# Kernel tuning notes

Hardware: AMD Instinct MI355X
Metric: run time of the kernel (lower is better)

Reference implementation:

```python
import jax, jax.numpy as jnp
import numpy as np

N_EMBD = 1024
N_HEAD = 16
HEAD_DIM = N_EMBD // N_HEAD
B, T = 4, 2048


def setup_inputs() -> dict:
    key = jax.random.key(0)
    ks = jax.random.split(key, 5)
    s_in = 1.0 / np.sqrt(N_EMBD)
    return {
        "x": jax.random.normal(ks[0], (B, T, N_EMBD), dtype=jnp.float32),
        "w_attn": jax.random.normal(ks[1], (N_EMBD, 3 * N_EMBD), dtype=jnp.float32) * s_in,
        "b_attn": jnp.zeros((3 * N_EMBD,), dtype=jnp.float32),
        "w_proj": jax.random.normal(ks[2], (N_EMBD, N_EMBD), dtype=jnp.float32) * s_in,
        "b_proj": jnp.zeros((N_EMBD,), dtype=jnp.float32),
    }


def reference(x, w_attn, b_attn, w_proj, b_proj):
    b, t, c = x.shape
    qkv = x @ w_attn + b_attn                      # [B,T,3C]
    q, k, v = jnp.split(qkv, 3, axis=-1)
    # [B,T,C] -> [B,H,T,D]
    def heads(z):
        return z.reshape(b, t, N_HEAD, HEAD_DIM).transpose(0, 2, 1, 3)
    q, k, v = heads(q), heads(k), heads(v)
    scale = 1.0 / np.sqrt(HEAD_DIM)
    att = jnp.einsum("bhqd,bhkd->bhqk", q, k) * scale
    causal = jnp.tril(jnp.ones((t, t), dtype=bool))
    att = jnp.where(causal, att, -jnp.inf)
    att = jax.nn.softmax(att, axis=-1)
    y = jnp.einsum("bhqk,bhkd->bhqd", att, v)      # [B,H,T,D]
    y = y.transpose(0, 2, 1, 3).reshape(b, t, c)
    return y @ w_proj + b_proj
```

## Files before the change

kernel.cpp:

```cpp
#include <hip/hip_runtime.h>
#include <hip/hip_bf16.h>

#define B_  4
#define T_  2048
#define C_  1024
#define H_  16
#define D_  64
#define C3_ 3072

typedef __attribute__((ext_vector_type(8))) short bf16x8;
typedef __attribute__((ext_vector_type(4))) float f32x4;
typedef unsigned short u16;

#define CSCALE 0.1803368801111204f

__device__ __forceinline__ u16 f2bf(float f) {
  union { float f; unsigned int u; } v; v.f = f;
  unsigned int r = (v.u + 0x7FFFu + ((v.u >> 16) & 1u)) >> 16;
  return (u16)r;
}

__device__ __forceinline__ void gload16(void* l, const void* g) {
  __builtin_amdgcn_global_load_lds(
      (const __attribute__((address_space(1))) unsigned int*)g,
      (__attribute__((address_space(3))) unsigned int*)l, 16, 0, 0);
}

__global__ __launch_bounds__(256)
void cvt_bf16(const float* __restrict__ in, u16* __restrict__ out, int n8) {
  int i = blockIdx.x * 256 + threadIdx.x;
  if (i >= n8) return;
  float4 a = *(const float4*)(in + (size_t)i * 8);
  float4 b = *(const float4*)(in + (size_t)i * 8 + 4);
  ushort4 lo, hi;
  lo.x = f2bf(a.x); lo.y = f2bf(a.y); lo.z = f2bf(a.z); lo.w = f2bf(a.w);
  hi.x = f2bf(b.x); hi.y = f2bf(b.y); hi.z = f2bf(b.z); hi.w = f2bf(b.w);
  *(ushort4*)(out + (size_t)i * 8) = lo;
  *(ushort4*)(out + (size_t)i * 8 + 4) = hi;
}

__global__ __launch_bounds__(256)
void transcvt(const float* __restrict__ w, u16* __restrict__ wT, int K, int N) {
  int n  = blockIdx.x * 64 + (threadIdx.x & 63);
  int k0 = blockIdx.y * 16 + (threadIdx.x >> 6) * 4;
  float v0 = w[(size_t)(k0 + 0) * N + n];
  float v1 = w[(size_t)(k0 + 1) * N + n];
  float v2 = w[(size_t)(k0 + 2) * N + n];
  float v3 = w[(size_t)(k0 + 3) * N + n];
  ushort4 o; o.x = f2bf(v0); o.y = f2bf(v1); o.z = f2bf(v2); o.w = f2bf(v3);
  *(ushort4*)(wT + (size_t)n * K + k0) = o;
}

__global__ __launch_bounds__(256)
void vtrans(const u16* __restrict__ qkv, u16* __restrict__ vT) {
  const int bid = blockIdx.x;
  const int bh = bid >> 6, tc = bid & 63;
  const int d = threadIdx.x & 63, t4 = threadIdx.x >> 6;
  const int t8 = tc * 4 + t4;
  const int b = bh >> 4, h = bh & 15;
  const u16* src = qkv + (size_t)(b * T_ + t8 * 8) * C3_ + 2 * C_ + h * 64 + d;
  union { u16 a[8]; int4 v; } u;
#pragma unroll
  for (int e = 0; e < 8; ++e) u.a[e] = src[(size_t)e * C3_];
  *(int4*)(vT + ((size_t)bh * 64 + d) * T_ + t8 * 8) = u.v;
}

template <typename OutT>
__global__ __launch_bounds__(256)
void gemm_bf16(const u16* __restrict__ A, const u16* __restrict__ Bt,
               const float* __restrict__ bias, OutT* __restrict__ C,
               int M, int N, int K, int qscale_cols) {
  __shared__ int4 As4[512];
  __shared__ int4 Bs4[512];

  const int tid  = threadIdx.x;
  const int lane = tid & 63;
  const int wid  = tid >> 6;
  const int wr   = wid >> 1, wc = wid & 1;
  const int row0 = blockIdx.y * 128, col0 = blockIdx.x * 128;

  f32x4 acc[4][4];
#pragma unroll
  for (int m = 0; m < 4; ++m)
#pragma unroll
    for (int n = 0; n < 4; ++n) acc[m][n] = (f32x4){0.f, 0.f, 0.f, 0.f};

  const int L1 = tid, L2 = 256 + tid;
  const u16* a1 = A + (size_t)(row0 + ((L1 >> 6) * 16) + (L1 & 15)) * K + ((L1 >> 4) & 3) * 8;
  const u16* a2 = A + (size_t)(row0 + ((L2 >> 6) * 16) + (L2 & 15)) * K + ((L2 >> 4) & 3) * 8;
  const u16* b1 = Bt + (size_t)(col0 + ((L1 >> 6) * 16) + (L1 & 15)) * K + ((L1 >> 4) & 3) * 8;
  const u16* b2 = Bt + (size_t)(col0 + ((L2 >> 6) * 16) + (L2 & 15)) * K + ((L2 >> 4) & 3) * 8;

  const int nk = K >> 5;
  for (int kt = 0; kt < nk; ++kt) {
    __syncthreads();
    gload16(As4 + wid * 64, a1);
    gload16(As4 + 256 + wid * 64, a2);
    gload16(Bs4 + wid * 64, b1);
    gload16(Bs4 + 256 + wid * 64, b2);
    a1 += 32; a2 += 32; b1 += 32; b2 += 32;
    __syncthreads();

    bf16x8 a[4], b[4];
#pragma unroll
    for (int m = 0; m < 4; ++m)
      a[m] = *(const bf16x8*)(As4 + (wr * 4 + m) * 64 + lane);
#pragma unroll
    for (int n = 0; n < 4; ++n)
      b[n] = *(const bf16x8*)(Bs4 + (wc * 4 + n) * 64 + lane);
#pragma unroll
    for (int m = 0; m < 4; ++m)
#pragma unroll
      for (int n = 0; n < 4; ++n)
        acc[m][n] = __builtin_amdgcn_mfma_f32_16x16x32_bf16(a[m], b[n], acc[m][n], 0, 0, 0);
  }

  const int cc = lane & 15, qg = lane >> 4;
#pragma unroll
  for (int m = 0; m < 4; ++m) {
#pragma unroll
    for (int n = 0; n < 4; ++n) {
      const int gc = col0 + wc * 64 + n * 16 + cc;
      const float bv = bias[gc];
      const float sc = (gc < qscale_cols) ? CSCALE : 1.0f;
#pragma unroll
      for (int r = 0; r < 4; ++r) {
        const int gr = row0 + wr * 64 + m * 16 + qg * 4 + r;
        float val = (acc[m][n][r] + bv) * sc;
        if constexpr (sizeof(OutT) == 2)
          ((u16*)C)[(size_t)gr * N + gc] = f2bf(val);
        else
          ((float*)C)[(size_t)gr * N + gc] = val;
      }
    }
  }
}

__global__ __launch_bounds__(512, 4)
void attn_mfma(const u16* __restrict__ qkv, const u16* __restrict__ vT,
               u16* __restrict__ yout) {
  __shared__ int4 Ks4[512];
  __shared__ int4 Vs4[512];
  __shared__ int4 Ps4[2048];

  const int n   = blockIdx.x;
  const int xcd = n & 7, t = n >> 3;
  const int bh  = xcd * 8 + (t >> 3);
  const int ip  = t & 7;
  const int b   = bh >> 4, h = bh & 15;

  const int tid = threadIdx.x;
  const int lane = tid & 63, wq = tid >> 6;
  const int sub = wq & 3;
  const int cc = lane & 15, qg = lane >> 4;

  const int qt128 = (wq < 4) ? ip : (15 - ip);
  const int qrow0 = qt128 * 128 + sub * 32;
  const int diag  = qt128 * 2 + (sub >> 1);
  const int jn    = 32 - 2 * ip;

  const u16* kbase = qkv + (size_t)b * T_ * C3_ + C_ + h * D_;
  const u16* vtb   = vT + (size_t)bh * D_ * T_;

  bf16x8 qf[2][2];
#pragma unroll
  for (int hf = 0; hf < 2; ++hf) {
    const u16* qb = qkv + (size_t)(b * T_ + qrow0 + hf * 16 + cc) * C3_ + h * D_;
    qf[hf][0] = *(const bf16x8*)(qb + qg * 8);
    qf[hf][1] = *(const bf16x8*)(qb + 32 + qg * 8);
  }

  const u16* kg = kbase + (size_t)((tid >> 7) * 16 + (tid & 15)) * C3_ +
                  ((tid >> 6) & 1) * 32 + ((tid >> 4) & 3) * 8;
  const u16* vg = vtb + (size_t)((tid >> 7) * 16 + (tid & 15)) * T_ +
                  ((tid >> 6) & 1) * 32 + ((tid >> 4) & 3) * 8;

  int4 kpref = *(const int4*)kg;
  int4 vpref = *(const int4*)vg;

  float m_r[2] = {-1e30f, -1e30f}, l_r[2] = {0.f, 0.f};
  f32x4 o[2][4];
#pragma unroll
  for (int hf = 0; hf < 2; ++hf)
#pragma unroll
    for (int db = 0; db < 4; ++db) o[hf][db] = (f32x4){0.f, 0.f, 0.f, 0.f};

  for (int j = 0; j < jn; ++j) {
    __syncthreads();
    Ks4[tid] = kpref;
    Vs4[tid] = vpref;
    __syncthreads();
    if (j + 1 < jn) {
      kpref = *(const int4*)(kg + (size_t)(j + 1) * 64 * C3_);
      vpref = *(const int4*)(vg + (j + 1) * 64);
    }
    if (j > diag) continue;

    __builtin_amdgcn_s_setprio(1);
    f32x4 s[2][4];
#pragma unroll
    for (int kb = 0; kb < 4; ++kb) {
      bf16x8 kf0 = *(const bf16x8*)(Ks4 + kb * 128 + lane);
      bf16x8 kf1 = *(const bf16x8*)(Ks4 + kb * 128 + 64 + lane);
#pragma unroll
      for (int hf = 0; hf < 2; ++hf) {
        f32x4 z = (f32x4){0.f, 0.f, 0.f, 0.f};
        z = __builtin_amdgcn_mfma_f32_16x16x32_bf16(kf0, qf[hf][0], z, 0, 0, 0);
        z = __builtin_amdgcn_mfma_f32_16x16x32_bf16(kf1, qf[hf][1], z, 0, 0, 0);
        s[hf][kb] = z;
      }
    }
    __builtin_amdgcn_s_setprio(0);

    if (j == diag) {
#pragma unroll
      for (int hf = 0; hf < 2; ++hf) {
        const int qabs = qrow0 + hf * 16 + cc;
#pragma unroll
        for (int kb = 0; kb < 4; ++kb)
#pragma unroll
          for (int r = 0; r < 4; ++r)
            if ((j * 64 + kb * 16 + qg * 4 + r) > qabs) s[hf][kb][r] = -1e30f;
      }
    }

#pragma unroll
    for (int hf = 0; hf < 2; ++hf) {
      float mx = s[hf][0][0];
#pragma unroll
      for (int kb = 0; kb < 4; ++kb)
#pragma unroll
        for (int r = 0; r < 4; ++r) mx = fmaxf(mx, s[hf][kb][r]);
      mx = fmaxf(mx, __shfl_xor(mx, 16));
      mx = fmaxf(mx, __shfl_xor(mx, 32));

      if (!__all(mx <= m_r[hf])) {
        float mn = fmaxf(m_r[hf], mx);
        float al = exp2f(m_r[hf] - mn);
        m_r[hf] = mn;
        l_r[hf] *= al;
        float alq[4];
#pragma unroll
        for (int r = 0; r < 4; ++r)
          alq[r] = __shfl(al, (lane & 48) | (qg * 4 + r));
#pragma unroll
        for (int db = 0; db < 4; ++db)
#pragma unroll
          for (int r = 0; r < 4; ++r) o[hf][db][r] *= alq[r];
      }

      float lsum = 0.f;
#pragma unroll
      for (int kb = 0; kb < 4; ++kb)
#pragma unroll
        for (int r = 0; r < 4; ++r) {
          float p = exp2f(s[hf][kb][r] - m_r[hf]);
          s[hf][kb][r] = p;
          lsum += p;
        }
      l_r[hf] += lsum;

      char* myPb = (char*)(Ps4 + wq * 256 + hf * 128);
#pragma unroll
      for (int kb = 0; kb < 4; ++kb) {
        unsigned plo, phi;
        asm("v_cvt_pk_bf16_f32 %0, %1, %2" : "=v"(plo) : "v"(s[hf][kb][0]), "v"(s[hf][kb][1]));
        asm("v_cvt_pk_bf16_f32 %0, %1, %2" : "=v"(phi) : "v"(s[hf][kb][2]), "v"(s[hf][kb][3]));
        const int kv0 = kb * 16 + qg * 4;
        const int g = ((kv0 >> 5) << 6) + (((kv0 >> 3) & 3) << 4) + cc;
        uint2 pk; pk.x = plo; pk.y = phi;
        *(uint2*)(myPb + g * 16 + (kv0 & 7) * 2) = pk;
      }
    }

    bf16x8 pa[2][2];
#pragma unroll
    for (int hf = 0; hf < 2; ++hf)
#pragma unroll
      for (int ks = 0; ks < 2; ++ks)
        pa[hf][ks] = *(const bf16x8*)(Ps4 + wq * 256 + hf * 128 + ks * 64 + lane);
    __builtin_amdgcn_s_setprio(1);
#pragma unroll
    for (int db = 0; db < 4; ++db) {
#pragma unroll
      for (int ks = 0; ks < 2; ++ks) {
        bf16x8 vf = *(const bf16x8*)(Vs4 + db * 128 + ks * 64 + lane);
        o[0][db] = __builtin_amdgcn_mfma_f32_16x16x32_bf16(pa[0][ks], vf, o[0][db], 0, 0, 0);
        o[1][db] = __builtin_amdgcn_mfma_f32_16x16x32_bf16(pa[1][ks], vf, o[1][db], 0, 0, 0);
      }
    }
    __builtin_amdgcn_s_setprio(0);
  }

#pragma unroll
  for (int hf = 0; hf < 2; ++hf) {
    float ls = l_r[hf];
    ls += __shfl_xor(ls, 16);
    ls += __shfl_xor(ls, 32);
    float linv_l = 1.0f / ls;
    float linv[4];
#pragma unroll
    for (int r = 0; r < 4; ++r)
      linv[r] = __shfl(linv_l, (lane & 48) | (qg * 4 + r));

    u16* yb = yout + (size_t)(b * T_ + qrow0 + hf * 16 + qg * 4) * C_ + h * D_ + cc;
#pragma unroll
    for (int db = 0; db < 4; ++db)
#pragma unroll
      for (int r = 0; r < 4; ++r)
        yb[(size_t)r * C_ + db * 16] = f2bf(o[hf][db][r] * linv[r]);
  }
}

extern "C" void kernel_launch(void* const* d_in, const int* in_sizes, int n_in,
                              void* d_out, int out_size, void* d_ws, size_t ws_size,
                              hipStream_t stream) {
  const float* x      = (const float*)d_in[0];
  const float* w_attn = (const float*)d_in[1];
  const float* b_attn = (const float*)d_in[2];
  const float* w_proj = (const float*)d_in[3];
  const float* b_proj = (const float*)d_in[4];
  float* out = (float*)d_out;

  char* ws = (char*)d_ws;
  u16* xb  = (u16*)(ws);
  u16* waT = (u16*)(ws + 16777216);
  u16* wpT = (u16*)(ws + 23068672);
  u16* qkv = (u16*)(ws + 25165824);
  u16* yb  = (u16*)(ws + 75497472);
  u16* vT  = (u16*)(ws + 92274688);

  cvt_bf16<<<4096, 256, 0, stream>>>(x, xb, (B_ * T_ * C_) / 8);
  transcvt<<<dim3(C3_ / 64, C_ / 16), 256, 0, stream>>>(w_attn, waT, C_, C3_);
  transcvt<<<dim3(C_ / 64, C_ / 16), 256, 0, stream>>>(w_proj, wpT, C_, C_);

  gemm_bf16<u16><<<dim3(C3_ / 128, (B_ * T_) / 128), 256, 0, stream>>>(
      xb, waT, b_attn, qkv, B_ * T_, C3_, C_, C_);

  vtrans<<<4096, 256, 0, stream>>>(qkv, vT);

  attn_mfma<<<dim3(8 * H_ * B_), 512, 0, stream>>>(qkv, vT, yb);

  gemm_bf16<float><<<dim3(C_ / 128, (B_ * T_) / 128), 256, 0, stream>>>(
      yb, wpT, b_proj, out, B_ * T_, C_, C_, 0);
}
```

Before: 248.1 us.

## Replace 128x128 GEMM with double-buffered 256x256 ping-pong pipelined GEMM

```diff
diff --git a/kernel.cpp b/kernel.cpp
--- a/kernel.cpp
+++ b/kernel.cpp
@@ -66,67 +66,201 @@
 }
 
 template <typename OutT>
-__global__ __launch_bounds__(256)
-void gemm_bf16(const u16* __restrict__ A, const u16* __restrict__ Bt,
-               const float* __restrict__ bias, OutT* __restrict__ C,
-               int M, int N, int K, int qscale_cols) {
-  __shared__ int4 As4[512];
-  __shared__ int4 Bs4[512];
-
-  const int tid  = threadIdx.x;
-  const int lane = tid & 63;
-  const int wid  = tid >> 6;
-  const int wr   = wid >> 1, wc = wid & 1;
-  const int row0 = blockIdx.y * 128, col0 = blockIdx.x * 128;
-
-  f32x4 acc[4][4];
-#pragma unroll
-  for (int m = 0; m < 4; ++m)
-#pragma unroll
-    for (int n = 0; n < 4; ++n) acc[m][n] = (f32x4){0.f, 0.f, 0.f, 0.f};
-
-  const int L1 = tid, L2 = 256 + tid;
-  const u16* a1 = A + (size_t)(row0 + ((L1 >> 6) * 16) + (L1 & 15)) * K + ((L1 >> 4) & 3) * 8;
-  const u16* a2 = A + (size_t)(row0 + ((L2 >> 6) * 16) + (L2 & 15)) * K + ((L2 >> 4) & 3) * 8;
-  const u16* b1 = Bt + (size_t)(col0 + ((L1 >> 6) * 16) + (L1 & 15)) * K + ((L1 >> 4) & 3) * 8;
-  const u16* b2 = Bt + (size_t)(col0 + ((L2 >> 6) * 16) + (L2 & 15)) * K + ((L2 >> 4) & 3) * 8;
-
-  const int nk = K >> 5;
-  for (int kt = 0; kt < nk; ++kt) {
-    __syncthreads();
-    gload16(As4 + wid * 64, a1);
-    gload16(As4 + 256 + wid * 64, a2);
-    gload16(Bs4 + wid * 64, b1);
-    gload16(Bs4 + 256 + wid * 64, b2);
-    a1 += 32; a2 += 32; b1 += 32; b2 += 32;
-    __syncthreads();
-
-    bf16x8 a[4], b[4];
-#pragma unroll
-    for (int m = 0; m < 4; ++m)
-      a[m] = *(const bf16x8*)(As4 + (wr * 4 + m) * 64 + lane);
-#pragma unroll
-    for (int n = 0; n < 4; ++n)
-      b[n] = *(const bf16x8*)(Bs4 + (wc * 4 + n) * 64 + lane);
-#pragma unroll
-    for (int m = 0; m < 4; ++m)
-#pragma unroll
-      for (int n = 0; n < 4; ++n)
-        acc[m][n] = __builtin_amdgcn_mfma_f32_16x16x32_bf16(a[m], b[n], acc[m][n], 0, 0, 0);
+__global__ __launch_bounds__(512, 2)
+void gemm256(const u16* __restrict__ A, const u16* __restrict__ Bt,
+             const float* __restrict__ bias, OutT* __restrict__ C,
+             int M, int N, int K, int qscale_cols) {
+  __shared__ int4 lds[8192];
+
+  const int tid = threadIdx.x, lane = tid & 63, wid = tid >> 6;
+  const int wr = wid >> 2, wc = wid & 3;
+  const int row0 = blockIdx.y * 256, col0 = blockIdx.x * 256;
+
+  f32x4 acc[8][4];
+#pragma unroll
+  for (int m = 0; m < 8; ++m)
+#pragma unroll
+    for (int nf = 0; nf < 4; ++nf) acc[m][nf] = (f32x4){0.f, 0.f, 0.f, 0.f};
+
+  const u16* pA[2][2]; const u16* pB[2][2];
+#pragma unroll
+  for (int h = 0; h < 2; ++h)
+#pragma unroll
+    for (int i = 0; i < 2; ++i) {
+      int g = h * 1024 + i * 512 + tid;
+      int rr = ((g >> 7) << 4) + (g & 15), ko = ((g >> 4) & 7) * 8;
+      pA[h][i] = A + (size_t)(row0 + rr) * K + ko;
+      pB[h][i] = Bt + (size_t)(col0 + rr) * K + ko;
+    }
+
+  auto stage = [&](int t, int isA, int h, int buf) {
+    const u16* p0 = (isA ? pA[h][0] : pB[h][0]) + t * 64;
+    const u16* p1 = (isA ? pA[h][1] : pB[h][1]) + t * 64;
+    int4* d = &lds[buf * 4096 + (isA ? 0 : 2048) + h * 1024 + wid * 64];
+    gload16(d, p0);
+    gload16(d + 512, p1);
+  };
+  auto rdA = [&](int f, int kk, int buf) {
+    return *(const bf16x8*)&lds[buf * 4096 + (wr * 8 + f) * 128 + kk * 64 + lane];
+  };
+  auto rdB = [&](int nf, int kk, int buf) {
+    return *(const bf16x8*)&lds[buf * 4096 + 2048 + (wc * 4 + nf) * 128 + kk * 64 + lane];
+  };
+
+  const int nk = K >> 6, nit = nk >> 1;
+
+  stage(0, 1, 0, 0); stage(0, 1, 1, 0); stage(0, 0, 0, 0); stage(0, 0, 1, 0);
+  stage(1, 0, 0, 1); stage(1, 0, 1, 1); stage(1, 1, 0, 1);
+  asm volatile("s_waitcnt vmcnt(6)" ::: "memory");
+  __builtin_amdgcn_s_barrier();
+
+  for (int it = 0; it < nit; ++it) {
+    const int t1g = 2 * it + 1, t2g = t1g + 1, t3g = t1g + 2;
+    bf16x8 a0[4][2], a1[4][2], b0[2][2], b1[2][2];
+
+#pragma unroll
+    for (int m = 0; m < 4; ++m) { a0[m][0] = rdA(m, 0, 0); a0[m][1] = rdA(m, 1, 0); }
+#pragma unroll
+    for (int nf = 0; nf < 2; ++nf) { b0[nf][0] = rdB(nf, 0, 0); b0[nf][1] = rdB(nf, 1, 0); }
+    stage(t1g, 1, 1, 1);
+    __builtin_amdgcn_s_barrier();
+    __builtin_amdgcn_s_setprio(1);
+#pragma unroll
+    for (int m = 0; m < 4; ++m)
+#pragma unroll
+      for (int nf = 0; nf < 2; ++nf) {
+        acc[m][nf] = __builtin_amdgcn_mfma_f32_16x16x32_bf16(a0[m][0], b0[nf][0], acc[m][nf], 0, 0, 0);
+        acc[m][nf] = __builtin_amdgcn_mfma_f32_16x16x32_bf16(a0[m][1], b0[nf][1], acc[m][nf], 0, 0, 0);
+      }
+    __builtin_amdgcn_s_setprio(0);
+    __builtin_amdgcn_s_barrier();
+
+#pragma unroll
+    for (int nf = 0; nf < 2; ++nf) { b1[nf][0] = rdB(2 + nf, 0, 0); b1[nf][1] = rdB(2 + nf, 1, 0); }
+    __builtin_amdgcn_s_barrier();
+    __builtin_amdgcn_s_setprio(1);
+#pragma unroll
+    for (int m = 0; m < 4; ++m)
+#pragma unroll
+      for (int nf = 0; nf < 2; ++nf) {
+        acc[m][2 + nf] = __builtin_amdgcn_mfma_f32_16x16x32_bf16(a0[m][0], b1[nf][0], acc[m][2 + nf], 0, 0, 0);
+        acc[m][2 + nf] = __builtin_amdgcn_mfma_f32_16x16x32_bf16(a0[m][1], b1[nf][1], acc[m][2 + nf], 0, 0, 0);
+      }
+    __builtin_amdgcn_s_setprio(0);
+    __builtin_amdgcn_s_barrier();
+
+#pragma unroll
+    for (int m = 0; m < 4; ++m) { a1[m][0] = rdA(4 + m, 0, 0); a1[m][1] = rdA(4 + m, 1, 0); }
+    if (t2g < nk) stage(t2g, 0, 0, 0);
+    __builtin_amdgcn_s_barrier();
+    __builtin_amdgcn_s_setprio(1);
+#pragma unroll
+    for (int m = 0; m < 4; ++m)
+#pragma unroll
+      for (int nf = 0; nf < 2; ++nf) {
+        acc[4 + m][2 + nf] = __builtin_amdgcn_mfma_f32_16x16x32_bf16(a1[m][0], b1[nf][0], acc[4 + m][2 + nf], 0, 0, 0);
+        acc[4 + m][2 + nf] = __builtin_amdgcn_mfma_f32_16x16x32_bf16(a1[m][1], b1[nf][1], acc[4 + m][2 + nf], 0, 0, 0);
+      }
+    __builtin_amdgcn_s_setprio(0);
+    __builtin_amdgcn_s_barrier();
+
+    if (t2g < nk) {
+      stage(t2g, 0, 1, 0);
+      stage(t2g, 1, 0, 0);
+      asm volatile("s_waitcnt vmcnt(6)" ::: "memory");
+    } else {
+      asm volatile("s_waitcnt vmcnt(0)" ::: "memory");
+    }
+    __builtin_amdgcn_s_barrier();
+    __builtin_amdgcn_s_setprio(1);
+#pragma unroll
+    for (int m = 0; m < 4; ++m)
+#pragma unroll
+      for (int nf = 0; nf < 2; ++nf) {
+        acc[4 + m][nf] = __builtin_amdgcn_mfma_f32_16x16x32_bf16(a1[m][0], b0[nf][0], acc[4 + m][nf], 0, 0, 0);
+        acc[4 + m][nf] = __builtin_amdgcn_mfma_f32_16x16x32_bf16(a1[m][1], b0[nf][1], acc[4 + m][nf], 0, 0, 0);
+      }
+    __builtin_amdgcn_s_setprio(0);
+    __builtin_amdgcn_s_barrier();
+
+#pragma unroll
+    for (int m = 0; m < 4; ++m) { a0[m][0] = rdA(m, 0, 1); a0[m][1] = rdA(m, 1, 1); }
+#pragma unroll
+    for (int nf = 0; nf < 2; ++nf) { b0[nf][0] = rdB(nf, 0, 1); b0[nf][1] = rdB(nf, 1, 1); }
+    if (t2g < nk) stage(t2g, 1, 1, 0);
+    __builtin_amdgcn_s_barrier();
+    __builtin_amdgcn_s_setprio(1);
+#pragma unroll
+    for (int m = 0; m < 4; ++m)
+#pragma unroll
+      for (int nf = 0; nf < 2; ++nf) {
+        acc[m][nf] = __builtin_amdgcn_mfma_f32_16x16x32_bf16(a0[m][0], b0[nf][0], acc[m][nf], 0, 0, 0);
+        acc[m][nf] = __builtin_amdgcn_mfma_f32_16x16x32_bf16(a0[m][1], b0[nf][1], acc[m][nf], 0, 0, 0);
+      }
+    __builtin_amdgcn_s_setprio(0);
+    __builtin_amdgcn_s_barrier();
+
+#pragma unroll
+    for (int nf = 0; nf < 2; ++nf) { b1[nf][0] = rdB(2 + nf, 0, 1); b1[nf][1] = rdB(2 + nf, 1, 1); }
+    __builtin_amdgcn_s_barrier();
+    __builtin_amdgcn_s_setprio(1);
+#pragma unroll
+    for (int m = 0; m < 4; ++m)
+#pragma unroll
+      for (int nf = 0; nf < 2; ++nf) {
+        acc[m][2 + nf] = __builtin_amdgcn_mfma_f32_16x16x32_bf16(a0[m][0], b1[nf][0], acc[m][2 + nf], 0, 0, 0);
+        acc[m][2 + nf] = __builtin_amdgcn_mfma_f32_16x16x32_bf16(a0[m][1], b1[nf][1], acc[m][2 + nf], 0, 0, 0);
+      }
+    __builtin_amdgcn_s_setprio(0);
+    __builtin_amdgcn_s_barrier();
+
+#pragma unroll
+    for (int m = 0; m < 4; ++m) { a1[m][0] = rdA(4 + m, 0, 1); a1[m][1] = rdA(4 + m, 1, 1); }
+    if (t3g < nk) stage(t3g, 0, 0, 1);
+    __builtin_amdgcn_s_barrier();
+    __builtin_amdgcn_s_setprio(1);
+#pragma unroll
+    for (int m = 0; m < 4; ++m)
+#pragma unroll
+      for (int nf = 0; nf < 2; ++nf) {
+        acc[4 + m][2 + nf] = __builtin_amdgcn_mfma_f32_16x16x32_bf16(a1[m][0], b1[nf][0], acc[4 + m][2 + nf], 0, 0, 0);
+        acc[4 + m][2 + nf] = __builtin_amdgcn_mfma_f32_16x16x32_bf16(a1[m][1], b1[nf][1], acc[4 + m][2 + nf], 0, 0, 0);
+      }
+    __builtin_amdgcn_s_setprio(0);
+    __builtin_amdgcn_s_barrier();
+
+    if (t3g < nk) {
+      stage(t3g, 0, 1, 1);
+      stage(t3g, 1, 0, 1);
+      asm volatile("s_waitcnt vmcnt(6)" ::: "memory");
+    } else {
+      asm volatile("s_waitcnt vmcnt(0)" ::: "memory");
+    }
+    __builtin_amdgcn_s_barrier();
+    __builtin_amdgcn_s_setprio(1);
+#pragma unroll
+    for (int m = 0; m < 4; ++m)
+#pragma unroll
+      for (int nf = 0; nf < 2; ++nf) {
+        acc[4 + m][nf] = __builtin_amdgcn_mfma_f32_16x16x32_bf16(a1[m][0], b0[nf][0], acc[4 + m][nf], 0, 0, 0);
+        acc[4 + m][nf] = __builtin_amdgcn_mfma_f32_16x16x32_bf16(a1[m][1], b0[nf][1], acc[4 + m][nf], 0, 0, 0);
+      }
+    __builtin_amdgcn_s_setprio(0);
+    __builtin_amdgcn_s_barrier();
   }
 
   const int cc = lane & 15, qg = lane >> 4;
 #pragma unroll
-  for (int m = 0; m < 4; ++m) {
-#pragma unroll
-    for (int n = 0; n < 4; ++n) {
-      const int gc = col0 + wc * 64 + n * 16 + cc;
+  for (int m = 0; m < 8; ++m) {
+#pragma unroll
+    for (int nf = 0; nf < 4; ++nf) {
+      const int gc = col0 + wc * 64 + nf * 16 + cc;
       const float bv = bias[gc];
       const float sc = (gc < qscale_cols) ? CSCALE : 1.0f;
 #pragma unroll
       for (int r = 0; r < 4; ++r) {
-        const int gr = row0 + wr * 64 + m * 16 + qg * 4 + r;
-        float val = (acc[m][n][r] + bv) * sc;
+        const int gr = row0 + wr * 128 + m * 16 + qg * 4 + r;
+        float val = (acc[m][nf][r] + bv) * sc;
         if constexpr (sizeof(OutT) == 2)
           ((u16*)C)[(size_t)gr * N + gc] = f2bf(val);
         else
@@ -334,13 +468,13 @@
   transcvt<<<dim3(C3_ / 64, C_ / 16), 256, 0, stream>>>(w_attn, waT, C_, C3_);
   transcvt<<<dim3(C_ / 64, C_ / 16), 256, 0, stream>>>(w_proj, wpT, C_, C_);
 
-  gemm_bf16<u16><<<dim3(C3_ / 128, (B_ * T_) / 128), 256, 0, stream>>>(
+  gemm256<u16><<<dim3(C3_ / 256, (B_ * T_) / 256), 512, 0, stream>>>(
       xb, waT, b_attn, qkv, B_ * T_, C3_, C_, C_);
 
   vtrans<<<4096, 256, 0, stream>>>(qkv, vT);
 
   attn_mfma<<<dim3(8 * H_ * B_), 512, 0, stream>>>(qkv, vT, yb);
 
-  gemm_bf16<float><<<dim3(C_ / 128, (B_ * T_) / 128), 256, 0, stream>>>(
+  gemm256<float><<<dim3(C_ / 256, (B_ * T_) / 256), 512, 0, stream>>>(
       yb, wpT, b_proj, out, B_ * T_, C_, C_, 0);
 }
```

New measurement: 224.3 us. 1.11x faster.
